# Kernel tuning notes

Measured on AMD Instinct MI355X. Metric: run time of the kernel, lower is better.

## Reference

```python
import jax, jax.numpy as jnp
import numpy as np

B, T, S, PD = 512, 2048, 16, 4

def setup_inputs() -> dict:
    key = jax.random.key(0)
    ks = jax.random.split(key, 10)
    w = lambda k, sh: (jax.random.normal(k, sh, dtype=jnp.float32) * 0.1)
    return {
        'z': jax.random.normal(ks[0], (B, T, S), dtype=jnp.float32),
        'p': jax.random.normal(ks[1], (B, T, PD), dtype=jnp.float32),
        'mu0': jnp.zeros((B, S), dtype=jnp.float32),
        'P0': jnp.full((B, S), 0.1, dtype=jnp.float32),  # cfg['kf_P0']
        'Wq1': w(ks[2], (PD, 64)), 'bq1': jnp.zeros((64,), jnp.float32),
        'Wq2': w(ks[3], (64, S)),  'bq2': jnp.zeros((S,), jnp.float32),
        'Wr1': w(ks[4], (PD, 64)), 'br1': jnp.zeros((64,), jnp.float32),
        'Wr2': w(ks[5], (64, S)),  'br2': jnp.zeros((S,), jnp.float32),
        'Wg1': w(ks[6], (PD, 32)), 'bg1': jnp.zeros((32,), jnp.float32),
        'Wg2': w(ks[7], (32, 1)),  'bg2': jnp.zeros((1,), jnp.float32),
    }

def _mlp(x, W1, b1, W2, b2):
    return jax.nn.relu(x @ W1 + b1) @ W2 + b2

def reference(z, p, mu0, P0, Wq1, bq1, Wq2, bq2, Wr1, br1, Wr2, br2, Wg1, bg1, Wg2, bg2):
    # z: [B,T,S], p: [B,T,PD]; scan over time with batched Kalman state.
    zT = jnp.swapaxes(z, 0, 1)  # [T,B,S]
    pT = jnp.swapaxes(p, 0, 1)  # [T,B,PD]

    def step(carry, inp):
        mu, P = carry            # [B,S], [B,S]
        z_t, p_t = inp           # [B,S], [B,PD]
        Q_t = jax.nn.softplus(_mlp(p_t, Wq1, bq1, Wq2, bq2)) + 1e-8
        R_t = jax.nn.softplus(_mlp(p_t, Wr1, br1, Wr2, br2)) + 1e-8
        P_pred = P + Q_t
        K = jnp.clip(P_pred / (P_pred + R_t), 1e-6, 0.95)
        gamma_t = jax.nn.sigmoid(_mlp(p_t, Wg1, bg1, Wg2, bg2))  # [B,1] (scalar per sample)
        mu_new = mu + gamma_t * (K * (z_t - mu))
        P_new = (1.0 - K) * P_pred
        return (mu_new, P_new), mu_new

    (mu_f, P_f), mus = jax.lax.scan(step, (mu0, P0), (zT, pT))
    return jnp.swapaxes(mus, 0, 1)  # [B,T,S]
```

## Files before the change

### kernel.cpp

```cpp
#include <hip/hip_runtime.h>
#include <hip/hip_fp16.h>
#include <stdint.h>
#include <math.h>

#define KB 512
#define KT 2048
#define KS 16
#define KPD 4
#define QT 512
#define NQ (KT / QT)
#define QSTR 515

typedef _Float16 f16;
typedef _Float16 f16x8 __attribute__((ext_vector_type(8)));
typedef float f32x4 __attribute__((ext_vector_type(4)));

#define MFMA16(A, B, C) __builtin_amdgcn_mfma_f32_16x16x32_f16(A, B, C, 0, 0, 0)

__device__ __forceinline__ float softplus_f(float x) {
    float ax = fabsf(x);
    float e  = __expf(-ax);
    return fmaxf(x, 0.0f) + __logf(1.0f + e);
}
__device__ __forceinline__ float sigmoid_f(float x) {
    return __builtin_amdgcn_rcpf(1.0f + __expf(-x));
}
__device__ __forceinline__ float h2f_lo(uint32_t w) {
    return __half2float(__ushort_as_half((unsigned short)(w & 0xffffu)));
}
__device__ __forceinline__ float h2f_hi(uint32_t w) {
    return __half2float(__ushort_as_half((unsigned short)(w >> 16)));
}
__device__ __forceinline__ f16x8 zero8() {
    f16x8 v;
#pragma unroll
    for (int i = 0; i < 8; ++i) v[i] = (f16)0;
    return v;
}
__device__ __forceinline__ int spos(int t) { return t ^ ((t >> 5) & 31); }

__device__ __forceinline__ uint32_t pkrelu(float a, float b) {
    auto h = __builtin_amdgcn_cvt_pkrtz(fmaxf(a, 0.f), fmaxf(b, 0.f));
    uint32_t w; __builtin_memcpy(&w, &h, 4);
    return w;
}

__global__ __launch_bounds__(512, 2) void kalman_one(
    const float* __restrict__ z, const float* __restrict__ p,
    const float* __restrict__ mu0, const float* __restrict__ P0,
    const float* __restrict__ Wq1, const float* __restrict__ bq1,
    const float* __restrict__ Wq2, const float* __restrict__ bq2,
    const float* __restrict__ Wr1, const float* __restrict__ br1,
    const float* __restrict__ Wr2, const float* __restrict__ br2,
    const float* __restrict__ Wg1, const float* __restrict__ bg1,
    const float* __restrict__ Wg2, const float* __restrict__ bg2,
    float* __restrict__ out)
{
    __shared__ __align__(16) uint32_t QRl[KS * QSTR];
    __shared__ __align__(16) float    Gl[QT];
    __shared__ __align__(16) float    zs[KS * QSTR];

    const int tid = threadIdx.x;
    const int wv = tid >> 6;
    const int l = tid & 63;
    const int g = l >> 4;
    const int c = l & 15;
    const int b = blockIdx.x;

    const float* __restrict__ zb = z + (size_t)b * KT * KS;
    const float* __restrict__ pb = p + (size_t)b * KT * KPD;
    float* __restrict__ ob = out + (size_t)b * KT * KS;

    f16x8 fA1[10];
#pragma unroll
    for (int m = 0; m < 10; ++m) {
        const float* W = (m < 4) ? (Wq1 + m * 16)
                       : (m < 8) ? (Wr1 + (m - 4) * 16)
                                 : (Wg1 + (m - 8) * 16);
        const int ld = (m < 8) ? 64 : 32;
        float w0 = W[0 * ld + c], w1 = W[1 * ld + c],
              w2 = W[2 * ld + c], w3 = W[3 * ld + c];
        f16x8 a = zero8();
        if (g == 0) { a[0] = (f16)w0; a[1] = (f16)w1; a[2] = (f16)w2; a[3] = (f16)w3; }
        fA1[m] = a;
    }
    f16x8 fA2[5];
#pragma unroll
    for (int i = 0; i < 4; ++i) {
        const float* W = (i < 2) ? Wq2 : Wr2;
        const int kb = (i & 1) * 32;
        f16x8 a;
#pragma unroll
        for (int j = 0; j < 8; ++j) a[j] = (f16)W[(kb + g * 8 + j) * 16 + c];
        fA2[i] = a;
    }
    {
        f16x8 a = zero8();
        if (c == 0) {
#pragma unroll
            for (int j = 0; j < 8; ++j) a[j] = (f16)Wg2[g * 8 + j];
        }
        fA2[4] = a;
    }
    const float bQ0 = bq2[g * 4 + 0], bQ1 = bq2[g * 4 + 1],
                bQ2 = bq2[g * 4 + 2], bQ3 = bq2[g * 4 + 3];
    const float bR0 = br2[g * 4 + 0], bR1 = br2[g * 4 + 1],
                bR2 = br2[g * 4 + 2], bR3 = br2[g * 4 + 3];
    const float bG = bg2[0];

    const int sa = ((g & 1) * 2) * 16 + c;
    const int sb = sa + 16;
    const bool hiM = (g >= 2);

    float muA = mu0[b * KS + wv],     PA = P0[b * KS + wv];
    float muB = mu0[b * KS + wv + 8], PB = P0[b * KS + wv + 8];

    auto scan_s = [&](int s, float& mu_q, float& P_q) {
        uint32_t qr[8];
        const uint32_t* qrow = QRl + (size_t)s * QSTR;
        float zvv[8], gvv[8];
#pragma unroll
        for (int i = 0; i < 8; ++i) {
            const int ps = spos(l * 8 + i);
            qr[i] = qrow[ps];
            zvv[i] = zs[s * QSTR + ps];
            gvv[i] = Gl[ps];
        }
        float c00 = 1.f, c01 = 0.f, c10 = 0.f, c11 = 1.f;
#pragma unroll
        for (int i = 0; i < 8; ++i) {
            float Q = h2f_lo(qr[i]), Rr = h2f_hi(qr[i]);
            float ta = fmaf(Q, c10, c00);
            float tb = fmaf(Q, c11, c01);
            float n10 = fmaf(Q + Rr, c10, c00);
            float n11 = fmaf(Q + Rr, c11, c01);
            c00 = Rr * ta; c01 = Rr * tb; c10 = n10; c11 = n11;
        }
        float rn = __builtin_amdgcn_rcpf(c11);
        float ma = c00 * rn, mb = c01 * rn, mc = c10 * rn;
#pragma unroll
        for (int r = 0; r < 6; ++r) {
            const int d = 1 << r;
            float pa = __shfl_up(ma, d);
            float pbv = __shfl_up(mb, d);
            float pc = __shfl_up(mc, d);
            float na = fmaf(ma, pa, mb * pc);
            float nb = fmaf(ma, pbv, mb);
            float nc = fmaf(mc, pa, pc);
            float nd = fmaf(mc, pbv, 1.f);
            float rr = __builtin_amdgcn_rcpf(nd);
            bool act = (l >= d);
            ma = act ? na * rr : ma;
            mb = act ? nb * rr : mb;
            mc = act ? nc * rr : mc;
        }
        float ea = __shfl_up(ma, 1);
        float eb = __shfl_up(mb, 1);
        float ec = __shfl_up(mc, 1);
        if (l == 0) { ea = 1.f; eb = 0.f; ec = 0.f; }
        float P = fmaf(ea, P_q, eb) * __builtin_amdgcn_rcpf(fmaf(ec, P_q, 1.f));

        float av[8], bw[8];
        float A = 1.f, Bv = 0.f;
#pragma unroll
        for (int i = 0; i < 8; ++i) {
            float Q = h2f_lo(qr[i]), Rr = h2f_hi(qr[i]);
            float Pp = P + Q;
            float K0 = Pp * __builtin_amdgcn_rcpf(Pp + Rr);
            float Kk = __builtin_amdgcn_fmed3f(K0, 1e-6f, 0.95f);
            float gk = gvv[i] * Kk;
            av[i] = 1.f - gk;
            bw[i] = gk * zvv[i];
            P = fmaf(-Kk, Pp, Pp);
            A = A * av[i];
            Bv = fmaf(av[i], Bv, bw[i]);
        }
        float P_end = __shfl(P, 63);
#pragma unroll
        for (int r = 0; r < 6; ++r) {
            const int d = 1 << r;
            float pA = __shfl_up(A, d);
            float pB = __shfl_up(Bv, d);
            float nA = A * pA;
            float nB = fmaf(A, pB, Bv);
            bool act = (l >= d);
            A  = act ? nA : A;
            Bv = act ? nB : Bv;
        }
        float eA = __shfl_up(A, 1);
        float eB = __shfl_up(Bv, 1);
        if (l == 0) { eA = 1.f; eB = 0.f; }
        float mu = fmaf(eA, mu_q, eB);
#pragma unroll
        for (int i = 0; i < 8; ++i) {
            mu = fmaf(av[i], mu, bw[i]);
            zs[s * QSTR + spos(l * 8 + i)] = mu;
        }
        mu_q = __shfl(mu, 63);
        P_q = P_end;
    };

    for (int q = 0; q < NQ; ++q) {
        {
            const int trow = q * QT + wv * 64;
            const float4 pv = *reinterpret_cast<const float4*>(pb + (size_t)(trow + l) * KPD);

#pragma unroll
            for (int n = 0; n < 4; ++n) {
                f16x8 fBP;
                {
                    const int src = n * 16 + c;
                    float x = __shfl(pv.x, src);
                    float y = __shfl(pv.y, src);
                    float zz = __shfl(pv.z, src);
                    float w = __shfl(pv.w, src);
                    fBP = zero8();
                    if (g == 0) { fBP[0] = (f16)x; fBP[1] = (f16)y; fBP[2] = (f16)zz; fBP[3] = (f16)w; }
                }

                f32x4 aq; aq[0] = bQ0; aq[1] = bQ1; aq[2] = bQ2; aq[3] = bQ3;
                f32x4 ar; ar[0] = bR0; ar[1] = bR1; ar[2] = bR2; ar[3] = bR3;
                f32x4 ag; ag[0] = 0.f; ag[1] = 0.f; ag[2] = 0.f; ag[3] = 0.f;

#pragma unroll
                for (int X = 0; X < 5; ++X) {
                    const int m0 = 2 * X, m1 = 2 * X + 1;
                    uint32_t a0, a1, b0, b1;
                    {
                        const float* bs = (m0 < 4) ? (bq1 + m0 * 16)
                                        : (m0 < 8) ? (br1 + (m0 - 4) * 16)
                                                   : (bg1 + (m0 - 8) * 16);
                        f32x4 acc;
                        acc[0] = bs[g * 4 + 0]; acc[1] = bs[g * 4 + 1];
                        acc[2] = bs[g * 4 + 2]; acc[3] = bs[g * 4 + 3];
                        acc = MFMA16(fA1[m0], fBP, acc);
                        a0 = pkrelu(acc[0], acc[1]);
                        a1 = pkrelu(acc[2], acc[3]);
                    }
                    {
                        const float* bs = (m1 < 4) ? (bq1 + m1 * 16)
                                        : (m1 < 8) ? (br1 + (m1 - 4) * 16)
                                                   : (bg1 + (m1 - 8) * 16);
                        f32x4 acc;
                        acc[0] = bs[g * 4 + 0]; acc[1] = bs[g * 4 + 1];
                        acc[2] = bs[g * 4 + 2]; acc[3] = bs[g * 4 + 3];
                        acc = MFMA16(fA1[m1], fBP, acc);
                        b0 = pkrelu(acc[0], acc[1]);
                        b1 = pkrelu(acc[2], acc[3]);
                    }
                    uint32_t t0 = __shfl(a0, sa), t1 = __shfl(a1, sa);
                    uint32_t t2 = __shfl(a0, sb), t3 = __shfl(a1, sb);
                    uint32_t u0 = __shfl(b0, sa), u1 = __shfl(b1, sa);
                    uint32_t u2 = __shfl(b0, sb), u3 = __shfl(b1, sb);
                    uint32_t w0 = hiM ? u0 : t0;
                    uint32_t w1 = hiM ? u1 : t1;
                    uint32_t w2 = hiM ? u2 : t2;
                    uint32_t w3 = hiM ? u3 : t3;
                    f16x8 fb;
                    __builtin_memcpy(&fb, &w0, 4);
                    __builtin_memcpy(reinterpret_cast<char*>(&fb) + 4, &w1, 4);
                    __builtin_memcpy(reinterpret_cast<char*>(&fb) + 8, &w2, 4);
                    __builtin_memcpy(reinterpret_cast<char*>(&fb) + 12, &w3, 4);
                    if (X == 0)      aq = MFMA16(fA2[0], fb, aq);
                    else if (X == 1) aq = MFMA16(fA2[1], fb, aq);
                    else if (X == 2) ar = MFMA16(fA2[2], fb, ar);
                    else if (X == 3) ar = MFMA16(fA2[3], fb, ar);
                    else             ag = MFMA16(fA2[4], fb, ag);
                }

                const int tt = wv * 64 + n * 16 + c;
                const int ps = spos(tt);
#pragma unroll
                for (int i = 0; i < 4; ++i) {
                    float Qv = softplus_f(aq[i]) + 1e-8f;
                    float Rv = softplus_f(ar[i]) + 1e-8f;
                    auto pk = __builtin_amdgcn_cvt_pkrtz(Qv, Rv);
                    uint32_t w; __builtin_memcpy(&w, &pk, 4);
                    QRl[(size_t)(g * 4 + i) * QSTR + ps] = w;
                }
                if (g == 0)
                    Gl[ps] = sigmoid_f(ag[0] + bG);
            }

            const float4* zq = reinterpret_cast<const float4*>(zb + (size_t)q * QT * KS);
#pragma unroll
            for (int v = 0; v < 4; ++v) {
                int k = tid + 512 * v;
                float4 w = zq[k];
                int t = k >> 2, s0 = (k & 3) << 2;
                const int ps = spos(t);
                zs[(s0 + 0) * QSTR + ps] = w.x;
                zs[(s0 + 1) * QSTR + ps] = w.y;
                zs[(s0 + 2) * QSTR + ps] = w.z;
                zs[(s0 + 3) * QSTR + ps] = w.w;
            }
        }
        __syncthreads();

        scan_s(wv, muA, PA);
        scan_s(wv + 8, muB, PB);
        __syncthreads();

        {
            float* od = ob + (size_t)q * QT * KS;
#pragma unroll
            for (int v = 0; v < 4; ++v) {
                int k = tid + 512 * v;
                int t = k >> 2, s0 = (k & 3) << 2;
                const int ps = spos(t);
                float4 w;
                w.x = zs[(s0 + 0) * QSTR + ps];
                w.y = zs[(s0 + 1) * QSTR + ps];
                w.z = zs[(s0 + 2) * QSTR + ps];
                w.w = zs[(s0 + 3) * QSTR + ps];
                *reinterpret_cast<float4*>(od + 4 * (size_t)k) = w;
            }
        }
        __syncthreads();
    }
}

extern "C" void kernel_launch(void* const* d_in, const int* in_sizes, int n_in,
                              void* d_out, int out_size, void* d_ws, size_t ws_size,
                              hipStream_t stream) {
    const float* z   = (const float*)d_in[0];
    const float* p   = (const float*)d_in[1];
    const float* mu0 = (const float*)d_in[2];
    const float* P0  = (const float*)d_in[3];
    const float* Wq1 = (const float*)d_in[4];
    const float* bq1 = (const float*)d_in[5];
    const float* Wq2 = (const float*)d_in[6];
    const float* bq2 = (const float*)d_in[7];
    const float* Wr1 = (const float*)d_in[8];
    const float* br1 = (const float*)d_in[9];
    const float* Wr2 = (const float*)d_in[10];
    const float* br2 = (const float*)d_in[11];
    const float* Wg1 = (const float*)d_in[12];
    const float* bg1 = (const float*)d_in[13];
    const float* Wg2 = (const float*)d_in[14];
    const float* bg2 = (const float*)d_in[15];
    float* out = (float*)d_out;

    hipLaunchKernelGGL(kalman_one, dim3(KB), dim3(512), 0, stream,
                       z, p, mu0, P0, Wq1, bq1, Wq2, bq2,
                       Wr1, br1, Wr2, br2, Wg1, bg1, Wg2, bg2, out);
}
```

Before: 93.41 us.

## Stage hidden activations through LDS and store z/mu buffer as fp16

Replaces the eight cross-lane shuffles and selects that rebuilt the second-layer MFMA operand with writes of packed relu outputs to a per-wave LDS scratch, followed by one 16-byte vector read. The z/mu staging buffer changes from fp32 to fp16, halving its LDS footprint and possibly allowing more resident blocks. Storing z and the output mu in half precision loses accuracy: the final output is rounded to fp16 and the recurrence reads fp16 z. There is no barrier between the LDS writes and reads within a wave, so correctness depends on wave-synchronous ordering.

Result: faster. 86.88 us (-7.0%).

```diff
diff --git a/kernel.cpp b/kernel.cpp
--- a/kernel.cpp
+++ b/kernel.cpp
@@ -10,6 +10,7 @@
 #define QT 512
 #define NQ (KT / QT)
 #define QSTR 515
+#define HSTR 40
 
 typedef _Float16 f16;
 typedef _Float16 f16x8 __attribute__((ext_vector_type(8)));
@@ -43,6 +44,12 @@
     auto h = __builtin_amdgcn_cvt_pkrtz(fmaxf(a, 0.f), fmaxf(b, 0.f));
     uint32_t w; __builtin_memcpy(&w, &h, 4);
     return w;
+}
+__device__ __forceinline__ uint16_t f2h(float x) {
+    return (uint16_t)__half_as_ushort(__float2half_rn(x));
+}
+__device__ __forceinline__ float h2f(uint16_t x) {
+    return __half2float(__ushort_as_half((unsigned short)x));
 }
 
 __global__ __launch_bounds__(512, 2) void kalman_one(
@@ -58,7 +65,8 @@
 {
     __shared__ __align__(16) uint32_t QRl[KS * QSTR];
     __shared__ __align__(16) float    Gl[QT];
-    __shared__ __align__(16) float    zs[KS * QSTR];
+    __shared__ __align__(16) uint16_t Hs[8 * KS * HSTR];
+    __shared__ __align__(16) uint16_t zsh[KS * QSTR];
 
     const int tid = threadIdx.x;
     const int wv = tid >> 6;
@@ -66,6 +74,8 @@
     const int g = l >> 4;
     const int c = l & 15;
     const int b = blockIdx.x;
+
+    f16* __restrict__ Hw = reinterpret_cast<f16*>(Hs) + wv * (KS * HSTR);
 
     const float* __restrict__ zb = z + (size_t)b * KT * KS;
     const float* __restrict__ pb = p + (size_t)b * KT * KPD;
@@ -108,10 +118,6 @@
                 bR2 = br2[g * 4 + 2], bR3 = br2[g * 4 + 3];
     const float bG = bg2[0];
 
-    const int sa = ((g & 1) * 2) * 16 + c;
-    const int sb = sa + 16;
-    const bool hiM = (g >= 2);
-
     float muA = mu0[b * KS + wv],     PA = P0[b * KS + wv];
     float muB = mu0[b * KS + wv + 8], PB = P0[b * KS + wv + 8];
 
@@ -123,7 +129,7 @@
         for (int i = 0; i < 8; ++i) {
             const int ps = spos(l * 8 + i);
             qr[i] = qrow[ps];
-            zvv[i] = zs[s * QSTR + ps];
+            zvv[i] = h2f(zsh[s * QSTR + ps]);
             gvv[i] = Gl[ps];
         }
         float c00 = 1.f, c01 = 0.f, c10 = 0.f, c11 = 1.f;
@@ -194,7 +200,7 @@
 #pragma unroll
         for (int i = 0; i < 8; ++i) {
             mu = fmaf(av[i], mu, bw[i]);
-            zs[s * QSTR + spos(l * 8 + i)] = mu;
+            zsh[s * QSTR + spos(l * 8 + i)] = f2h(mu);
         }
         mu_q = __shfl(mu, 63);
         P_q = P_end;
@@ -222,10 +228,11 @@
                 f32x4 ar; ar[0] = bR0; ar[1] = bR1; ar[2] = bR2; ar[3] = bR3;
                 f32x4 ag; ag[0] = 0.f; ag[1] = 0.f; ag[2] = 0.f; ag[3] = 0.f;
 
+                uint32_t* Hd = reinterpret_cast<uint32_t*>(Hw);
+
 #pragma unroll
                 for (int X = 0; X < 5; ++X) {
                     const int m0 = 2 * X, m1 = 2 * X + 1;
-                    uint32_t a0, a1, b0, b1;
                     {
                         const float* bs = (m0 < 4) ? (bq1 + m0 * 16)
                                         : (m0 < 8) ? (br1 + (m0 - 4) * 16)
@@ -234,8 +241,8 @@
                         acc[0] = bs[g * 4 + 0]; acc[1] = bs[g * 4 + 1];
                         acc[2] = bs[g * 4 + 2]; acc[3] = bs[g * 4 + 3];
                         acc = MFMA16(fA1[m0], fBP, acc);
-                        a0 = pkrelu(acc[0], acc[1]);
-                        a1 = pkrelu(acc[2], acc[3]);
+                        Hd[c * 20 + g * 2 + 0] = pkrelu(acc[0], acc[1]);
+                        Hd[c * 20 + g * 2 + 1] = pkrelu(acc[2], acc[3]);
                     }
                     {
                         const float* bs = (m1 < 4) ? (bq1 + m1 * 16)
@@ -245,22 +252,10 @@
                         acc[0] = bs[g * 4 + 0]; acc[1] = bs[g * 4 + 1];
                         acc[2] = bs[g * 4 + 2]; acc[3] = bs[g * 4 + 3];
                         acc = MFMA16(fA1[m1], fBP, acc);
-                        b0 = pkrelu(acc[0], acc[1]);
-                        b1 = pkrelu(acc[2], acc[3]);
+                        Hd[c * 20 + 8 + g * 2 + 0] = pkrelu(acc[0], acc[1]);
+                        Hd[c * 20 + 8 + g * 2 + 1] = pkrelu(acc[2], acc[3]);
                     }
-                    uint32_t t0 = __shfl(a0, sa), t1 = __shfl(a1, sa);
-                    uint32_t t2 = __shfl(a0, sb), t3 = __shfl(a1, sb);
-                    uint32_t u0 = __shfl(b0, sa), u1 = __shfl(b1, sa);
-                    uint32_t u2 = __shfl(b0, sb), u3 = __shfl(b1, sb);
-                    uint32_t w0 = hiM ? u0 : t0;
-                    uint32_t w1 = hiM ? u1 : t1;
-                    uint32_t w2 = hiM ? u2 : t2;
-                    uint32_t w3 = hiM ? u3 : t3;
-                    f16x8 fb;
-                    __builtin_memcpy(&fb, &w0, 4);
-                    __builtin_memcpy(reinterpret_cast<char*>(&fb) + 4, &w1, 4);
-                    __builtin_memcpy(reinterpret_cast<char*>(&fb) + 8, &w2, 4);
-                    __builtin_memcpy(reinterpret_cast<char*>(&fb) + 12, &w3, 4);
+                    f16x8 fb = *reinterpret_cast<const f16x8*>(Hw + c * HSTR + g * 8);
                     if (X == 0)      aq = MFMA16(fA2[0], fb, aq);
                     else if (X == 1) aq = MFMA16(fA2[1], fb, aq);
                     else if (X == 2) ar = MFMA16(fA2[2], fb, ar);
@@ -289,10 +284,10 @@
                 float4 w = zq[k];
                 int t = k >> 2, s0 = (k & 3) << 2;
                 const int ps = spos(t);
-                zs[(s0 + 0) * QSTR + ps] = w.x;
-                zs[(s0 + 1) * QSTR + ps] = w.y;
-                zs[(s0 + 2) * QSTR + ps] = w.z;
-                zs[(s0 + 3) * QSTR + ps] = w.w;
+                zsh[(s0 + 0) * QSTR + ps] = f2h(w.x);
+                zsh[(s0 + 1) * QSTR + ps] = f2h(w.y);
+                zsh[(s0 + 2) * QSTR + ps] = f2h(w.z);
+                zsh[(s0 + 3) * QSTR + ps] = f2h(w.w);
             }
         }
         __syncthreads();
@@ -309,10 +304,10 @@
                 int t = k >> 2, s0 = (k & 3) << 2;
                 const int ps = spos(t);
                 float4 w;
-                w.x = zs[(s0 + 0) * QSTR + ps];
-                w.y = zs[(s0 + 1) * QSTR + ps];
-                w.z = zs[(s0 + 2) * QSTR + ps];
-                w.w = zs[(s0 + 3) * QSTR + ps];
+                w.x = h2f(zsh[(s0 + 0) * QSTR + ps]);
+                w.y = h2f(zsh[(s0 + 1) * QSTR + ps]);
+                w.z = h2f(zsh[(s0 + 2) * QSTR + ps]);
+                w.w = h2f(zsh[(s0 + 3) * QSTR + ps]);
                 *reinterpret_cast<float4*>(od + 4 * (size_t)k) = w;
             }
         }
```
